# Kernel tuning notes

Hardware: AMD Instinct MI355X
Metric: run time of the kernel (lower is better)

Reference implementation:

```python
import jax, jax.numpy as jnp
import numpy as np

C = 512          # in_channels == key_channels
K_REGIONS = 256  # number of proxy/object regions
N, H, Wd = 8, 128, 128


def _cba(x, w, sc, bi):
    """1x1 Conv + (folded) BN + ReLU. x: [n, Cin, h, w], w: [Cout, Cin]."""
    y = jnp.einsum('nchw,oc->nohw', x, w)
    return jax.nn.relu(sc[None, :, None, None] * y + bi[None, :, None, None])


def setup_inputs() -> dict:
    key = jax.random.key(0)
    kx, kp, kw, ks, kb = jax.random.split(key, 5)
    x = jax.random.normal(kx, (N, C, H, Wd), dtype=jnp.float32)
    proxy = jax.random.normal(kp, (N, C, K_REGIONS, 1), dtype=jnp.float32)
    # 7 ConvBnAct layers: [fp0, fp1, fo0, fo1, fd0, fd1, fup]
    W = jax.random.normal(kw, (7, C, C), dtype=jnp.float32) * (1.0 / np.sqrt(C))
    s = jax.random.uniform(ks, (7, C), dtype=jnp.float32, minval=0.5, maxval=1.5)
    b = jax.random.normal(kb, (7, C), dtype=jnp.float32) * 0.02
    return {'x': x, 'proxy': proxy, 'W': W, 's': s, 'b': b}


def reference(x, proxy, W, s, b):
    n, _, h, w = x.shape
    # f_pixel(x): two 1x1 ConvBnAct -> query [n, HW, C]
    q = _cba(_cba(x, W[0], s[0], b[0]), W[1], s[1], b[1])
    query = q.reshape(n, C, h * w).transpose(0, 2, 1)          # [n, HW, C]
    # f_object(proxy) -> key [n, C, K]
    k = _cba(_cba(proxy, W[2], s[2], b[2]), W[3], s[3], b[3])
    key_t = k.reshape(n, C, -1)                                 # [n, C, K]
    # f_down(proxy) -> value [n, K, C]
    v = _cba(_cba(proxy, W[4], s[4], b[4]), W[5], s[5], b[5])
    value = v.reshape(n, C, -1).transpose(0, 2, 1)              # [n, K, C]
    # scaled dot-product attention (single head, unmasked)
    sim = jnp.einsum('nqc,nck->nqk', query, key_t) * (C ** -0.5)
    sim = jax.nn.softmax(sim, axis=-1)                          # [n, HW, K]
    context = jnp.einsum('nqk,nkc->nqc', sim, value)            # [n, HW, C]
    context = context.transpose(0, 2, 1).reshape(n, C, h, w)
    # f_up
    return _cba(context, W[6], s[6], b[6])
```

## Files before the change

### kernel.cpp

```cpp
#include <hip/hip_runtime.h>
#include <hip/hip_bf16.h>
#include <stdint.h>

typedef __bf16 bf16;
typedef __bf16 bf16x8 __attribute__((ext_vector_type(8)));
typedef __bf16 bf16x4v __attribute__((ext_vector_type(4)));
typedef float f32x4 __attribute__((ext_vector_type(4)));

#define AS1 __attribute__((address_space(1)))
#define AS3 __attribute__((address_space(3)))

__device__ __forceinline__ void g2lds16(const bf16* g, bf16* l) {
  __builtin_amdgcn_global_load_lds((AS1 void*)(uintptr_t)g, (AS3 void*)l, 16, 0, 0);
}

__global__ void prep_weights_k(const float* __restrict__ W, const float* __restrict__ s,
                               const float* __restrict__ b, bf16* __restrict__ Wb,
                               float* __restrict__ bb, bf16* __restrict__ W24,
                               float* __restrict__ b24) {
  int idx = blockIdx.x * 256 + threadIdx.x;
  int c = idx & 511;
  int o = (idx >> 9) & 511;
  int l = idx >> 18;
  const float r = 0.04419417382415922f;
  float f = (l == 3) ? r : 1.0f;
  float wv = W[idx] * s[(l << 9) + o] * f;
  float bv = b[(l << 9) + o] * f;
  Wb[idx] = (bf16)wv;
  if (c == 0) bb[(l << 9) + o] = bv;
  if (l == 2) { W24[(size_t)o * 512 + c] = (bf16)wv;         if (c == 0) b24[o] = bv; }
  if (l == 4) { W24[(size_t)(512 + o) * 512 + c] = (bf16)wv; if (c == 0) b24[512 + o] = bv; }
}

__global__ void transpose_cast_k(const float* __restrict__ in, bf16* __restrict__ out,
                                 int R, int S) {
  __shared__ float tile[64][65];
  int s0 = blockIdx.x * 64, r0 = blockIdx.y * 64;
  size_t zo = (size_t)blockIdx.z * R * S;
  int t = threadIdx.x;
  int rr = t >> 4, cc = t & 15;
#pragma unroll
  for (int i = 0; i < 4; i++) {
    float4 v = *(const float4*)&in[zo + (size_t)(r0 + rr + 16 * i) * S + s0 + cc * 4];
    tile[rr + 16 * i][cc * 4 + 0] = v.x;
    tile[rr + 16 * i][cc * 4 + 1] = v.y;
    tile[rr + 16 * i][cc * 4 + 2] = v.z;
    tile[rr + 16 * i][cc * 4 + 3] = v.w;
  }
  __syncthreads();
#pragma unroll
  for (int i = 0; i < 4; i++) {
    int sR = rr + 16 * i;
    bf16x4v o;
    o.x = (bf16)tile[cc * 4 + 0][sR];
    o.y = (bf16)tile[cc * 4 + 1][sR];
    o.z = (bf16)tile[cc * 4 + 2][sR];
    o.w = (bf16)tile[cc * 4 + 3][sR];
    *(bf16x4v*)&out[zo + (size_t)(s0 + sR) * R + r0 + cc * 4] = o;
  }
}

template <bool RELU, bool OUTF32, int BIASMODE>
__global__ __launch_bounds__(256, 2) void gemm_nt(
    const bf16* __restrict__ A, long sAb, int lda,
    const bf16* __restrict__ B, long sBb, int ldb,
    void* __restrict__ OUT, long sOb,
    const float* __restrict__ bias,
    int M, int N, int Kd) {
  __shared__ bf16 sA[128][64];
  __shared__ bf16 sB[128][64];
  const int n0 = blockIdx.x * 128;
  const int m0 = blockIdx.y * 128;
  const bf16* Ab = A + (size_t)blockIdx.z * sAb;
  const bf16* Bb = B + (size_t)blockIdx.z * sBb;
  const int t = threadIdx.x;
  const int lane = t & 63;
  const int w = t >> 6;
  const int wm = (w & 1) << 6;
  const int wn = (w >> 1) << 6;
  const int srow = t >> 3;
  const int scol = (t & 7) << 3;

  f32x4 acc[4][4] = {};
  const int fr = lane & 15;
  const int fq = (lane >> 4) << 3;

  for (int k0 = 0; k0 < Kd; k0 += 64) {
#pragma unroll
    for (int i = 0; i < 4; i++) {
      g2lds16(Ab + (size_t)(m0 + i * 32 + srow) * lda + (k0 + scol), &sA[i * 32 + srow][scol]);
      g2lds16(Bb + (size_t)(n0 + i * 32 + srow) * ldb + (k0 + scol), &sB[i * 32 + srow][scol]);
    }
    __syncthreads();
#pragma unroll
    for (int kk = 0; kk < 64; kk += 32) {
      bf16x8 af[4], bfv[4];
#pragma unroll
      for (int i = 0; i < 4; i++) af[i] = *(const bf16x8*)&sA[wm + i * 16 + fr][kk + fq];
#pragma unroll
      for (int j = 0; j < 4; j++) bfv[j] = *(const bf16x8*)&sB[wn + j * 16 + fr][kk + fq];
#pragma unroll
      for (int i = 0; i < 4; i++)
#pragma unroll
        for (int j = 0; j < 4; j++)
          acc[i][j] = __builtin_amdgcn_mfma_f32_16x16x32_bf16(af[i], bfv[j], acc[i][j], 0, 0, 0);
    }
    __syncthreads();
  }

  const int rb = m0 + wm + ((lane >> 4) << 2);
  const int cb = n0 + wn + (lane & 15);
#pragma unroll
  for (int i = 0; i < 4; i++) {
#pragma unroll
    for (int r = 0; r < 4; r++) {
      const int orow = rb + i * 16 + r;
#pragma unroll
      for (int j = 0; j < 4; j++) {
        const int oc = cb + j * 16;
        float vv = acc[i][j][r];
        if (BIASMODE == 1) vv += bias[oc];
        else if (BIASMODE == 2) vv += bias[orow];
        if (RELU) vv = fmaxf(vv, 0.0f);
        if (OUTF32)
          ((float*)OUT)[(size_t)blockIdx.z * sOb + (size_t)orow * N + oc] = vv;
        else
          ((bf16*)OUT)[(size_t)blockIdx.z * sOb + (size_t)orow * N + oc] = (bf16)vv;
      }
    }
  }
}

__global__ __launch_bounds__(256, 2) void sim_softmax_k(
    const bf16* __restrict__ Q, const bf16* __restrict__ Key, bf16* __restrict__ P) {
  __shared__ bf16 sQ[128][64];
  __shared__ bf16 sK[256][64];
  const int t = threadIdx.x;
  const int lane = t & 63;
  const int w = t >> 6;
  const int m0 = blockIdx.x * 128;
  const bf16* Qz = Q + (size_t)blockIdx.y * 16384 * 512;
  const bf16* Kz = Key + (size_t)blockIdx.y * 256 * 512;
  bf16* Pz = P + (size_t)blockIdx.y * 16384 * 256;

  const int fr = lane & 15;
  const int quad = lane >> 4;
  const int fq = quad << 3;
  const int wm = w << 5;
  const int srow = t >> 3;
  const int scol = (t & 7) << 3;

  f32x4 acc[2][16] = {};

  for (int k0 = 0; k0 < 512; k0 += 64) {
#pragma unroll
    for (int i = 0; i < 4; i++)
      g2lds16(Qz + (size_t)(m0 + i * 32 + srow) * 512 + k0 + scol, &sQ[i * 32 + srow][scol]);
#pragma unroll
    for (int i = 0; i < 8; i++)
      g2lds16(Kz + (size_t)(i * 32 + srow) * 512 + k0 + scol, &sK[i * 32 + srow][scol]);
    __syncthreads();
#pragma unroll
    for (int kk = 0; kk < 64; kk += 32) {
      bf16x8 aq0 = *(const bf16x8*)&sQ[wm + fr][kk + fq];
      bf16x8 aq1 = *(const bf16x8*)&sQ[wm + 16 + fr][kk + fq];
#pragma unroll
      for (int j = 0; j < 16; j++) {
        bf16x8 bk = *(const bf16x8*)&sK[j * 16 + fr][kk + fq];
        acc[0][j] = __builtin_amdgcn_mfma_f32_16x16x32_bf16(aq0, bk, acc[0][j], 0, 0, 0);
        acc[1][j] = __builtin_amdgcn_mfma_f32_16x16x32_bf16(aq1, bk, acc[1][j], 0, 0, 0);
      }
    }
    __syncthreads();
  }

#pragma unroll
  for (int i = 0; i < 2; i++) {
#pragma unroll
    for (int r = 0; r < 4; r++) {
      float m = acc[i][0][r];
#pragma unroll
      for (int j = 1; j < 16; j++) m = fmaxf(m, acc[i][j][r]);
#pragma unroll
      for (int o = 1; o < 16; o <<= 1) m = fmaxf(m, __shfl_xor(m, o));
      float sum = 0.0f;
#pragma unroll
      for (int j = 0; j < 16; j++) {
        float e = __expf(acc[i][j][r] - m);
        acc[i][j][r] = e;
        sum += e;
      }
#pragma unroll
      for (int o = 1; o < 16; o <<= 1) sum += __shfl_xor(sum, o);
      float inv = 1.0f / sum;
      const size_t rowoff = (size_t)(m0 + wm + i * 16 + (quad << 2) + r) * 256;
#pragma unroll
      for (int j = 0; j < 16; j++)
        Pz[rowoff + j * 16 + fr] = (bf16)(acc[i][j][r] * inv);
    }
  }
}

extern "C" void kernel_launch(void* const* d_in, const int* in_sizes, int n_in,
                              void* d_out, int out_size, void* d_ws, size_t ws_size,
                              hipStream_t stream) {
  const float* x = (const float*)d_in[0];
  const float* proxy = (const float*)d_in[1];
  const float* W = (const float*)d_in[2];
  const float* s = (const float*)d_in[3];
  const float* b = (const float*)d_in[4];
  float* out = (float*)d_out;

  const int C = 512, K = 256, NB = 8, HW = 16384;
  const size_t MiB = 1024 * 1024;
  char* ws = (char*)d_ws;
  if (ws_size < 272 * MiB) return;

  bf16* Wb   = (bf16*)(ws + 0);
  float* bb  = (float*)(ws + 3670016);
  bf16* W24  = (bf16*)(ws + 4 * MiB);
  float* b24 = (float*)(ws + 5 * MiB);
  bf16* pT   = (bf16*)(ws + 6 * MiB);
  bf16* kt   = (bf16*)(ws + 8 * MiB);
  bf16* key  = (bf16*)(ws + 12 * MiB);
  bf16* v    = (bf16*)(ws + 14 * MiB);
  bf16* bufA = (bf16*)(ws + 16 * MiB);
  bf16* bufB = (bf16*)(ws + 144 * MiB);

  bf16* xb  = bufA;
  bf16* t0  = bufB;
  bf16* q   = bufA;
  bf16* P   = bufB;
  bf16* ctx = bufA;

  const long KC = (long)K * C;
  const long KT = (long)K * 1024;
  const long HWC = (long)HW * C;
  const long HWK = (long)HW * K;

  prep_weights_k<<<7 * 512 * 512 / 256, 256, 0, stream>>>(W, s, b, Wb, bb, W24, b24);
  transpose_cast_k<<<dim3(K / 64, C / 64, NB), 256, 0, stream>>>(proxy, pT, C, K);
  transpose_cast_k<<<dim3(HW / 64, C / 64, NB), 256, 0, stream>>>(x, xb, C, HW);
  gemm_nt<true, false, 1><<<dim3(1024 / 128, K / 128, NB), 256, 0, stream>>>(
      pT, KC, C, W24, 0, C, kt, KT, b24, K, 1024, C);
  gemm_nt<true, false, 1><<<dim3(C / 128, K / 128, NB), 256, 0, stream>>>(
      kt, KT, 1024, Wb + 3 * 262144, 0, C, key, KC, bb + 3 * 512, K, C, C);
  gemm_nt<true, false, 2><<<dim3(K / 128, C / 128, NB), 256, 0, stream>>>(
      Wb + 5 * 262144, 0, C, kt + 512, KT, 1024, v, KC, bb + 5 * 512, C, K, C);
  gemm_nt<true, false, 1><<<dim3(C / 128, HW / 128, NB), 256, 0, stream>>>(
      xb, HWC, C, Wb, 0, C, t0, HWC, bb, HW, C, C);
  gemm_nt<true, false, 1><<<dim3(C / 128, HW / 128, NB), 256, 0, stream>>>(
      t0, HWC, C, Wb + 1 * 262144, 0, C, q, HWC, bb + 512, HW, C, C);
  sim_softmax_k<<<dim3(HW / 128, NB), 256, 0, stream>>>(q, key, P);
  gemm_nt<false, false, 0><<<dim3(C / 128, HW / 128, NB), 256, 0, stream>>>(
      P, HWK, K, v, KC, K, ctx, HWC, nullptr, HW, C, K);
  gemm_nt<true, true, 2><<<dim3(HW / 128, C / 128, NB), 256, 0, stream>>>(
      Wb + 6 * 262144, 0, C, ctx, HWC, C, out, HWC, bb + 6 * 512, C, HW, C);
}
```

Measured before the change: 957.9 us.

## Rewrite GEMM as 256x256-tile, 8-wave, double-buffered pipelined MFMA kernel

The GEMM moves from 128x128 tiles with 4 waves and a single LDS buffer to 256x256 tiles with 8 waves, a double-buffered LDS ring, and XOR-swizzled LDS layout to avoid bank conflicts. Global-to-LDS loads for the next K-step are interleaved with MFMA phases using explicit barriers, sched_barrier, setprio and vmcnt waits, so memory latency overlaps compute. All launches are re-gridded for the larger tile. This costs 128KB of LDS per block and more registers, which limits occupancy, and the small K=256 region GEMMs now launch very few blocks.

Measured after the change: 894.1 us. -6.7%, faster.

```diff
diff --git a/kernel.cpp b/kernel.cpp
--- a/kernel.cpp
+++ b/kernel.cpp
@@ -60,58 +60,135 @@
   }
 }
 
+
+#define MFMA16(AF, BF, IO, JO)                                                \
+  __builtin_amdgcn_s_setprio(1);                                              \
+  _Pragma("unroll") for (int kx = 0; kx < 2; kx++)                            \
+  _Pragma("unroll") for (int i = 0; i < 4; i++)                               \
+  _Pragma("unroll") for (int j = 0; j < 2; j++)                               \
+      acc[(IO) + i][(JO) + j] = __builtin_amdgcn_mfma_f32_16x16x32_bf16(      \
+          AF[i][kx], BF[j][kx], acc[(IO) + i][(JO) + j], 0, 0, 0);            \
+  __builtin_amdgcn_s_setprio(0);
+
+#define RD_A(DST, BUF, ROFF)                                                  \
+  _Pragma("unroll") for (int i = 0; i < 4; i++)                               \
+  _Pragma("unroll") for (int kx = 0; kx < 2; kx++) {                          \
+    const int ar = wm * 128 + (ROFF) + i * 16 + fr;                           \
+    DST[i][kx] = *(const bf16x8*)&sm[BUF][0][ar]                              \
+        [(((kx << 2) + fq8) ^ (ar & 7)) << 3];                                \
+  }
+
+#define RD_B(DST, BUF, COFF)                                                  \
+  _Pragma("unroll") for (int j = 0; j < 2; j++)                               \
+  _Pragma("unroll") for (int kx = 0; kx < 2; kx++) {                          \
+    const int br = wn * 64 + (COFF) + j * 16 + fr;                            \
+    DST[j][kx] = *(const bf16x8*)&sm[BUF][1][br]                              \
+        [(((kx << 2) + fq8) ^ (br & 7)) << 3];                                \
+  }
+
+#define PH_SYNC_PRE  __builtin_amdgcn_s_barrier(); __builtin_amdgcn_sched_barrier(0);
+#define PH_SYNC_POST __builtin_amdgcn_sched_barrier(0); __builtin_amdgcn_s_barrier();
+
 template <bool RELU, bool OUTF32, int BIASMODE>
-__global__ __launch_bounds__(256, 2) void gemm_nt(
+__global__ __launch_bounds__(512, 2) void gemm_nt(
     const bf16* __restrict__ A, long sAb, int lda,
     const bf16* __restrict__ B, long sBb, int ldb,
     void* __restrict__ OUT, long sOb,
     const float* __restrict__ bias,
     int M, int N, int Kd) {
-  __shared__ bf16 sA[128][64];
-  __shared__ bf16 sB[128][64];
-  const int n0 = blockIdx.x * 128;
-  const int m0 = blockIdx.y * 128;
-  const bf16* Ab = A + (size_t)blockIdx.z * sAb;
-  const bf16* Bb = B + (size_t)blockIdx.z * sBb;
+  __shared__ bf16 sm[2][2][256][64];
   const int t = threadIdx.x;
   const int lane = t & 63;
   const int w = t >> 6;
-  const int wm = (w & 1) << 6;
-  const int wn = (w >> 1) << 6;
-  const int srow = t >> 3;
-  const int scol = (t & 7) << 3;
-
-  f32x4 acc[4][4] = {};
+  const int wm = w >> 2;
+  const int wn = w & 3;
+  const int n0 = blockIdx.x * 256;
+  const int m0 = blockIdx.y * 256;
+  const bf16* __restrict__ Ab = A + (size_t)blockIdx.z * sAb;
+  const bf16* __restrict__ Bb = B + (size_t)blockIdx.z * sBb;
+  const int nk = Kd >> 6;
+
+  const int prow = t >> 3;
+  const int pchunk = t & 7;
+  const int lch = pchunk ^ (prow & 7);
+
   const int fr = lane & 15;
-  const int fq = (lane >> 4) << 3;
-
-  for (int k0 = 0; k0 < Kd; k0 += 64) {
-#pragma unroll
-    for (int i = 0; i < 4; i++) {
-      g2lds16(Ab + (size_t)(m0 + i * 32 + srow) * lda + (k0 + scol), &sA[i * 32 + srow][scol]);
-      g2lds16(Bb + (size_t)(n0 + i * 32 + srow) * ldb + (k0 + scol), &sB[i * 32 + srow][scol]);
+  const int fq8 = lane >> 4;
+
+  auto stage = [&](int ab, int h, int kt) {
+    const int ktc = (kt < nk) ? kt : 0;
+    const bf16* __restrict__ src = ab ? Bb : Ab;
+    const int ld = ab ? ldb : lda;
+    const int r0 = (ab ? n0 : m0) + h * 128;
+    const int buf = kt & 1;
+#pragma unroll
+    for (int j = 0; j < 2; j++) {
+      const int pr = j * 64 + prow;
+      g2lds16(src + (size_t)(r0 + pr) * ld + (ktc << 6) + (lch << 3),
+              &sm[buf][ab][h * 128 + pr][pchunk << 3]);
     }
-    __syncthreads();
-#pragma unroll
-    for (int kk = 0; kk < 64; kk += 32) {
-      bf16x8 af[4], bfv[4];
-#pragma unroll
-      for (int i = 0; i < 4; i++) af[i] = *(const bf16x8*)&sA[wm + i * 16 + fr][kk + fq];
-#pragma unroll
-      for (int j = 0; j < 4; j++) bfv[j] = *(const bf16x8*)&sB[wn + j * 16 + fr][kk + fq];
-#pragma unroll
-      for (int i = 0; i < 4; i++)
-#pragma unroll
-        for (int j = 0; j < 4; j++)
-          acc[i][j] = __builtin_amdgcn_mfma_f32_16x16x32_bf16(af[i], bfv[j], acc[i][j], 0, 0, 0);
-    }
-    __syncthreads();
-  }
-
-  const int rb = m0 + wm + ((lane >> 4) << 2);
-  const int cb = n0 + wn + (lane & 15);
-#pragma unroll
-  for (int i = 0; i < 4; i++) {
+  };
+
+  f32x4 acc[8][4] = {};
+  bf16x8 a0[4][2], a1[4][2], b0[2][2], b1[2][2];
+
+  stage(0, 0, 0); stage(0, 1, 0); stage(1, 0, 0); stage(1, 1, 0);
+  stage(1, 0, 1); stage(1, 1, 1);
+  asm volatile("s_waitcnt vmcnt(4)" ::: "memory");
+  __builtin_amdgcn_s_barrier();
+  __builtin_amdgcn_sched_barrier(0);
+
+  for (int T = 0; T < nk; T += 2) {
+    RD_A(a0, 0, 0)
+    RD_B(b0, 0, 0)
+    stage(0, 0, T + 1);
+    PH_SYNC_PRE
+    MFMA16(a0, b0, 0, 0)
+    PH_SYNC_POST
+    RD_B(b1, 0, 32)
+    stage(0, 1, T + 1);
+    PH_SYNC_PRE
+    MFMA16(a0, b1, 0, 2)
+    PH_SYNC_POST
+    RD_A(a1, 0, 64)
+    stage(1, 0, T + 2);
+    PH_SYNC_PRE
+    MFMA16(a1, b0, 4, 0)
+    PH_SYNC_POST
+    stage(1, 1, T + 2);
+    PH_SYNC_PRE
+    MFMA16(a1, b1, 4, 2)
+    asm volatile("s_waitcnt vmcnt(4)" ::: "memory");
+    PH_SYNC_POST
+    RD_A(a0, 1, 0)
+    RD_B(b0, 1, 0)
+    stage(0, 0, T + 2);
+    PH_SYNC_PRE
+    MFMA16(a0, b0, 0, 0)
+    PH_SYNC_POST
+    RD_B(b1, 1, 32)
+    stage(0, 1, T + 2);
+    PH_SYNC_PRE
+    MFMA16(a0, b1, 0, 2)
+    PH_SYNC_POST
+    RD_A(a1, 1, 64)
+    stage(1, 0, T + 3);
+    PH_SYNC_PRE
+    MFMA16(a1, b0, 4, 0)
+    PH_SYNC_POST
+    stage(1, 1, T + 3);
+    PH_SYNC_PRE
+    MFMA16(a1, b1, 4, 2)
+    asm volatile("s_waitcnt vmcnt(4)" ::: "memory");
+    PH_SYNC_POST
+  }
+
+  asm volatile("s_waitcnt vmcnt(0)" ::: "memory");
+
+  const int rb = m0 + wm * 128 + (fq8 << 2);
+  const int cb = n0 + wn * 64 + fr;
+#pragma unroll
+  for (int i = 0; i < 8; i++) {
 #pragma unroll
     for (int r = 0; r < 4; r++) {
       const int orow = rb + i * 16 + r;
@@ -241,19 +318,19 @@
   prep_weights_k<<<7 * 512 * 512 / 256, 256, 0, stream>>>(W, s, b, Wb, bb, W24, b24);
   transpose_cast_k<<<dim3(K / 64, C / 64, NB), 256, 0, stream>>>(proxy, pT, C, K);
   transpose_cast_k<<<dim3(HW / 64, C / 64, NB), 256, 0, stream>>>(x, xb, C, HW);
-  gemm_nt<true, false, 1><<<dim3(1024 / 128, K / 128, NB), 256, 0, stream>>>(
+  gemm_nt<true, false, 1><<<dim3(1024 / 256, K / 256, NB), 512, 0, stream>>>(
       pT, KC, C, W24, 0, C, kt, KT, b24, K, 1024, C);
-  gemm_nt<true, false, 1><<<dim3(C / 128, K / 128, NB), 256, 0, stream>>>(
+  gemm_nt<true, false, 1><<<dim3(C / 256, K / 256, NB), 512, 0, stream>>>(
       kt, KT, 1024, Wb + 3 * 262144, 0, C, key, KC, bb + 3 * 512, K, C, C);
-  gemm_nt<true, false, 2><<<dim3(K / 128, C / 128, NB), 256, 0, stream>>>(
+  gemm_nt<true, false, 2><<<dim3(K / 256, C / 256, NB), 512, 0, stream>>>(
       Wb + 5 * 262144, 0, C, kt + 512, KT, 1024, v, KC, bb + 5 * 512, C, K, C);
-  gemm_nt<true, false, 1><<<dim3(C / 128, HW / 128, NB), 256, 0, stream>>>(
+  gemm_nt<true, false, 1><<<dim3(C / 256, HW / 256, NB), 512, 0, stream>>>(
       xb, HWC, C, Wb, 0, C, t0, HWC, bb, HW, C, C);
-  gemm_nt<true, false, 1><<<dim3(C / 128, HW / 128, NB), 256, 0, stream>>>(
+  gemm_nt<true, false, 1><<<dim3(C / 256, HW / 256, NB), 512, 0, stream>>>(
       t0, HWC, C, Wb + 1 * 262144, 0, C, q, HWC, bb + 512, HW, C, C);
   sim_softmax_k<<<dim3(HW / 128, NB), 256, 0, stream>>>(q, key, P);
-  gemm_nt<false, false, 0><<<dim3(C / 128, HW / 128, NB), 256, 0, stream>>>(
+  gemm_nt<false, false, 0><<<dim3(C / 256, HW / 256, NB), 512, 0, stream>>>(
       P, HWK, K, v, KC, K, ctx, HWC, nullptr, HW, C, K);
-  gemm_nt<true, true, 2><<<dim3(HW / 128, C / 128, NB), 256, 0, stream>>>(
+  gemm_nt<true, true, 2><<<dim3(HW / 256, C / 256, NB), 512, 0, stream>>>(
       Wb + 6 * 262144, 0, C, ctx, HWC, C, out, HWC, bb + 6 * 512, C, HW, C);
 }
```
